# Performance work log

Hardware: AMD Instinct MI355X
Metric: run time of the kernel (lower is better)

The kernel has to match this reference:

```python
import jax, jax.numpy as jnp
import numpy as np

D_MODEL = 1024
N_HEADS = 16
D_K = D_MODEL // N_HEADS  # 64
SCALE = 0.125             # attention_scale = 1/sqrt(d_k)
ROPE_BASE = 10000.0
NEG_INF = -1e30


def setup_inputs() -> dict:
    key = jax.random.key(0)
    k1, k2, k3 = jax.random.split(key, 3)
    B, S = 2, 2048
    x = jax.random.normal(k1, (B, S, D_MODEL), jnp.float32)
    # torch Linear(d_model, 3*d_model, bias=False): stored here as [in, out]
    w_qkv = jax.random.normal(k2, (D_MODEL, 3 * D_MODEL), jnp.float32) * (D_MODEL ** -0.5)
    w_o = jax.random.normal(k3, (D_MODEL, D_MODEL), jnp.float32) * (D_MODEL ** -0.5)
    return {"x": x, "w_qkv": w_qkv, "w_o": w_o}


def _rotary(x):
    # x: [B, H, S, D]; standard half-split rotary over sequence positions
    S, D = x.shape[2], x.shape[3]
    inv_freq = 1.0 / (ROPE_BASE ** (jnp.arange(0, D, 2, dtype=jnp.float32) / D))  # [D/2]
    freqs = jnp.arange(S, dtype=jnp.float32)[:, None] * inv_freq[None, :]          # [S, D/2]
    cos = jnp.cos(freqs)[None, None]  # [1,1,S,D/2]
    sin = jnp.sin(freqs)[None, None]
    x1, x2 = jnp.split(x, 2, axis=-1)
    return jnp.concatenate([x1 * cos + x2 * sin, -x1 * sin + x2 * cos], axis=-1).astype(x.dtype)


def reference(x, w_qkv, w_o):
    B, S, _ = x.shape
    qkv = x @ w_qkv                                        # [B,S,3*D_MODEL]
    qkv = qkv.reshape(B, S, 3, N_HEADS, D_K).transpose(2, 0, 3, 1, 4)  # [3,B,H,S,Dk]
    q, k, v = qkv[0], qkv[1], qkv[2]
    q = _rotary(q)
    k = _rotary(k)
    scores = jnp.einsum('bhqd,bhkd->bhqk', q, k) * SCALE   # [B,H,S,S]
    causal = jnp.tril(jnp.ones((S, S), dtype=bool))
    scores = jnp.where(causal, scores, NEG_INF)
    attn = jax.nn.softmax(scores, axis=-1)
    out = jnp.einsum('bhqk,bhkd->bhqd', attn, v)           # [B,H,S,Dk]
    out = out.transpose(0, 2, 1, 3).reshape(B, S, D_MODEL)
    return out @ w_o
```

## Files before the change

kernel.cpp:

```cpp
#include <hip/hip_runtime.h>

typedef short bf16x8 __attribute__((ext_vector_type(8)));
typedef short bf16x4 __attribute__((ext_vector_type(4)));
typedef float f32x4 __attribute__((ext_vector_type(4)));
typedef float f32x16 __attribute__((ext_vector_type(16)));
typedef int i32x4 __attribute__((ext_vector_type(4)));

#define DEVI static __device__ __forceinline__

DEVI unsigned short f2b(float f) {
  unsigned u = __float_as_uint(f);
  u += 0x7FFFu + ((u >> 16) & 1u);
  return (unsigned short)(u >> 16);
}

DEVI void gload16(const void* g, void* l) {
  __builtin_amdgcn_global_load_lds((const __attribute__((address_space(1))) void*)g,
                                   (__attribute__((address_space(3))) void*)l, 16, 0, 0);
}

DEVI void pl32swap(int a, int b, int& outa, int& outb) {
#if __has_builtin(__builtin_amdgcn_permlane32_swap)
  auto r = __builtin_amdgcn_permlane32_swap(a, b, false, false);
  outa = ((const int*)&r)[0];
  outb = ((const int*)&r)[1];
#else
  int bp = __shfl_xor(b, 32);
  int ap = __shfl_xor(a, 32);
  outa = (threadIdx.x & 32) ? bp : a;
  outb = (threadIdx.x & 32) ? b : ap;
#endif
}

DEVI float halfmax(float x) {
  int o0, o1;
  pl32swap(__float_as_int(x), __float_as_int(x), o0, o1);
  return fmaxf(__int_as_float(o0), __int_as_float(o1));
}
DEVI float halfsum(float x) {
  int o0, o1;
  pl32swap(__float_as_int(x), __float_as_int(x), o0, o1);
  return __int_as_float(o0) + __int_as_float(o1);
}

__global__ void rope_table_kernel(float2* __restrict__ cst) {
  int i = blockIdx.x * 256 + threadIdx.x;
  int s = i >> 5, j = i & 31;
  float inv = powf(10000.0f, -(float)j * (1.0f / 32.0f));
  float a = (float)s * inv;
  cst[i] = make_float2(cosf(a), sinf(a));
}

__global__ void cvt_x_kernel(const float* __restrict__ x, unsigned short* __restrict__ xb) {
  int i = blockIdx.x * 256 + threadIdx.x;
  float4 v = ((const float4*)x)[i];
  ushort4 o;
  o.x = f2b(v.x); o.y = f2b(v.y); o.z = f2b(v.z); o.w = f2b(v.w);
  ((ushort4*)xb)[i] = o;
}

__global__ void transpose2_kernel(const float* __restrict__ W1, unsigned short* __restrict__ WT1,
                                  const float* __restrict__ W2, unsigned short* __restrict__ WT2) {
  __shared__ float tile[32][33];
  int bx = blockIdx.x;
  const float* W; unsigned short* WT; int N;
  if (bx < 96) { W = W1; WT = WT1; N = 3072; }
  else         { W = W2; WT = WT2; N = 1024; bx -= 96; }
  const int K = 1024;
  int n0 = bx * 32, k0 = blockIdx.y * 32;
  int tx = threadIdx.x, ty = threadIdx.y;
#pragma unroll
  for (int i = 0; i < 32; i += 8)
    tile[ty + i][tx] = W[(size_t)(k0 + ty + i) * N + n0 + tx];
  __syncthreads();
#pragma unroll
  for (int i = 0; i < 32; i += 8)
    WT[(size_t)(n0 + ty + i) * K + k0 + tx] = f2b(tile[tx][ty + i]);
}

DEVI void gemm_mainloop(const unsigned short* __restrict__ A, const unsigned short* __restrict__ B,
                        unsigned short* As, unsigned short* Bs,
                        int m0, int n0, int lane, int wid, int wr, int wc,
                        f32x4 acc[4][4]) {
  const int srow = lane >> 3;
  const int scc = ((lane & 7) ^ srow) * 8;
  const int rx = lane & 7;
  auto stage = [&](int k0, int nb) {
    unsigned short* Ad = As + nb * 8192;
    unsigned short* Bd = Bs + nb * 8192;
#pragma unroll
    for (int i = 0; i < 4; ++i) {
      const int c = i * 4 + wid;
      const int row = c * 8 + srow;
      gload16(A + (size_t)(m0 + row) * 1024 + k0 + scc, (char*)Ad + c * 1024);
      gload16(B + (size_t)(n0 + row) * 1024 + k0 + scc, (char*)Bd + c * 1024);
    }
  };
  auto compute = [&](int nb) {
    const unsigned short* Ab = As + nb * 8192;
    const unsigned short* Bb = Bs + nb * 8192;
#pragma unroll
    for (int kk = 0; kk < 64; kk += 32) {
      const int cc = (((kk >> 3) + (lane >> 4)) ^ rx) * 8;
      bf16x8 a[4], b[4];
#pragma unroll
      for (int mi = 0; mi < 4; ++mi)
        a[mi] = *(const bf16x8*)&Ab[(wr * 64 + mi * 16 + (lane & 15)) * 64 + cc];
#pragma unroll
      for (int ni = 0; ni < 4; ++ni)
        b[ni] = *(const bf16x8*)&Bb[(wc * 64 + ni * 16 + (lane & 15)) * 64 + cc];
      __builtin_amdgcn_s_setprio(1);
#pragma unroll
      for (int mi = 0; mi < 4; ++mi)
#pragma unroll
        for (int ni = 0; ni < 4; ++ni)
          acc[mi][ni] = __builtin_amdgcn_mfma_f32_16x16x32_bf16(a[mi], b[ni], acc[mi][ni], 0, 0, 0);
      __builtin_amdgcn_s_setprio(0);
    }
  };
  stage(0, 0);
  stage(64, 1);
  for (int t = 0; t < 15; ++t) {
    asm volatile("s_waitcnt vmcnt(8)" ::: "memory");
    __builtin_amdgcn_s_barrier();
    compute(t & 1);
    __builtin_amdgcn_s_barrier();
    if (t < 14) stage((t + 2) * 64, t & 1);
  }
  asm volatile("s_waitcnt vmcnt(0)" ::: "memory");
  __builtin_amdgcn_s_barrier();
  compute(1);
}

__global__ __launch_bounds__(256, 2) void gemm_qkv_kernel(
    const unsigned short* __restrict__ Xb, const unsigned short* __restrict__ WT,
    const float2* __restrict__ cst,
    unsigned short* __restrict__ Qb, unsigned short* __restrict__ Kb,
    unsigned short* __restrict__ VTb) {
  __shared__ unsigned short As[2][8192];
  __shared__ unsigned short Bs[2][8192];
  const int lane = threadIdx.x & 63, wid = threadIdx.x >> 6;
  const int flat = blockIdx.y * 24 + blockIdx.x;
  const int nf = (flat & 7) * 96 + (flat >> 3);
  const int bx = nf % 24, by = nf / 24;
  const int m0 = by * 128, n0 = bx * 128;
  const int wr = wid >> 1, wc = wid & 1;
  f32x4 acc[4][4] = {};
  gemm_mainloop(Xb, WT, &As[0][0], &Bs[0][0], m0, n0, lane, wid, wr, wc, acc);

  __syncthreads();
  unsigned short* slab = (unsigned short*)((char*)&As[0][0] + wid * 9216);
  const int n_base = n0 + wc * 64;
  const int ty = n_base >> 10;
  const int h = (n_base & 1023) >> 6;
  const int qrow = (lane >> 4) << 2;
  const int l15 = lane & 15;
  const int rlane = lane >> 3, clane = lane & 7;
  const int rowg = m0 + wr * 64;
  const int s_half = rowg & 2047, bb = rowg >> 11;

  if (ty < 2) {
    unsigned short* dst = (ty == 0) ? Qb : Kb;
#pragma unroll
    for (int mi = 0; mi < 4; ++mi) {
      const int rl0 = mi * 16 + qrow;
#pragma unroll
      for (int r = 0; r < 4; ++r) {
#pragma unroll
        for (int ni = 0; ni < 2; ++ni) {
          const int j = ni * 16 + l15;
          const float2 cs = cst[(s_half + rl0 + r) * 32 + j];
          const float x1 = acc[mi][ni][r], x2 = acc[mi][ni + 2][r];
          slab[(rl0 + r) * 72 + j]      = f2b(x1 * cs.x + x2 * cs.y);
          slab[(rl0 + r) * 72 + j + 32] = f2b(-x1 * cs.y + x2 * cs.x);
        }
      }
    }
    unsigned short* dp = dst + ((size_t)(bb * 16 + h) * 2048 + s_half) * 64;
#pragma unroll
    for (int i = 0; i < 8; ++i) {
      const int row = i * 8 + rlane;
      const bf16x8 v = *(const bf16x8*)&slab[row * 72 + clane * 8];
      *(bf16x8*)&dp[row * 64 + clane * 8] = v;
    }
  } else {
#pragma unroll
    for (int mi = 0; mi < 4; ++mi) {
      const int rl0 = mi * 16 + qrow;
#pragma unroll
      for (int ni = 0; ni < 4; ++ni) {
        const int d = ni * 16 + l15;
#pragma unroll
        for (int r = 0; r < 4; ++r)
          slab[d * 72 + rl0 + r] = f2b(acc[mi][ni][r]);
      }
    }
    unsigned short* vp = VTb + (size_t)(bb * 16 + h) * 64 * 2048 + s_half;
#pragma unroll
    for (int i = 0; i < 8; ++i) {
      const int d = i * 8 + rlane;
      const bf16x8 v = *(const bf16x8*)&slab[d * 72 + clane * 8];
      *(bf16x8*)&vp[(size_t)d * 2048 + clane * 8] = v;
    }
  }
}

DEVI void stage128(const unsigned short* __restrict__ Kh, const unsigned short* __restrict__ Vh,
                   int kbase, unsigned char* buf, int tid) {
#pragma unroll
  for (int i = 0; i < 4; ++i) {
    const int T = tid + i * 512;
    const int g = T >> 10;
    const int rem = T & 1023;
    const int cidx = rem & 511;
    const int c = cidx >> 6;
    const int l = cidx & 63;
    unsigned char* dst = buf + (T & ~63) * 16;
    if (rem < 512)
      gload16(Kh + (size_t)(kbase + g * 64 + l) * 64 + c * 8, dst);
    else
      gload16(Vh + (size_t)l * 2048 + kbase + g * 64 + c * 8, dst);
  }
}

DEVI void build_pa(const f32x16& s, bf16x8& pa0, bf16x8& pa1) {
  int cw[8];
#pragma unroll
  for (int i = 0; i < 8; ++i)
    asm("v_cvt_pk_bf16_f32 %0, %1, %2" : "=v"(cw[i]) : "v"(s[2 * i]), "v"(s[2 * i + 1]));
  int a0, a1, b0, b1, a2, a3, b2, b3;
  pl32swap(cw[0], cw[2], a0, b0);
  pl32swap(cw[1], cw[3], a1, b1);
  pl32swap(cw[4], cw[6], a2, b2);
  pl32swap(cw[5], cw[7], a3, b3);
  pa0 = __builtin_bit_cast(bf16x8, (i32x4){a0, a1, b0, b1});
  pa1 = __builtin_bit_cast(bf16x8, (i32x4){a2, a3, b2, b3});
}

DEVI void attn_pair(const unsigned char* __restrict__ bufK, const unsigned char* __restrict__ bufV,
                    const bf16x8 qf[4], int kglob, bool diag1, int qg, int ln, int hi,
                    float& m2, float& l_run, f32x16& acc0, f32x16& acc1) {
  const float C = 0.125f * 1.44269504f;
  f32x16 s0 = {}, s1 = {};
  {
    const unsigned char* kb = bufK + hi * 1024 + ln * 16;
    bf16x8 k0[4], k1[4];
#pragma unroll
    for (int j = 0; j < 4; ++j) {
      k0[j] = *(const bf16x8*)(kb + j * 2048);
      k1[j] = *(const bf16x8*)(kb + j * 2048 + 512);
    }
    __builtin_amdgcn_s_setprio(1);
#pragma unroll
    for (int j = 0; j < 4; ++j) {
      s0 = __builtin_amdgcn_mfma_f32_32x32x16_bf16(k0[j], qf[j], s0, 0, 0, 0);
      s1 = __builtin_amdgcn_mfma_f32_32x32x16_bf16(k1[j], qf[j], s1, 0, 0, 0);
    }
    __builtin_amdgcn_s_setprio(0);
  }
  bf16x8 va[2][2], vb[2][2];
  {
    const unsigned char* vbase = bufV + hi * 1024 + ln * 16;
#pragma unroll
    for (int st = 0; st < 2; ++st)
#pragma unroll
      for (int p = 0; p < 2; ++p) {
        va[st][p] = *(const bf16x8*)(vbase + (4 * st + 2 * p) * 1024);
        vb[st][p] = *(const bf16x8*)(vbase + (4 * st + 2 * p) * 1024 + 512);
      }
  }

  if (diag1) {
#pragma unroll
    for (int r = 0; r < 16; ++r) {
      const int kg = kglob + 32 + (r & 3) + ((r >> 2) << 3) + (hi << 2);
      if (kg > qg) s1[r] = -1e30f;
    }
  }
  float mraw = fmaxf(s0[0], s1[0]);
#pragma unroll
  for (int r = 1; r < 16; ++r) mraw = fmaxf(mraw, fmaxf(s0[r], s1[r]));
  const float mlc = mraw * C;
  if (__any(mlc > m2 + 11.5416f)) {
    const float mnew = fmaxf(m2, halfmax(mlc));
    const float sc = exp2f(m2 - mnew);
    l_run *= sc;
#pragma unroll
    for (int r = 0; r < 16; ++r) { acc0[r] *= sc; acc1[r] *= sc; }
    m2 = mnew;
  }
  float ps0 = 0.f, ps1 = 0.f;
#pragma unroll
  for (int r = 0; r < 16; ++r) { s0[r] = exp2f(fmaf(s0[r], C, -m2)); ps0 += s0[r]; }
#pragma unroll
  for (int r = 0; r < 16; ++r) { s1[r] = exp2f(fmaf(s1[r], C, -m2)); ps1 += s1[r]; }
  l_run += ps0 + ps1;

  bf16x8 pa[2][2];
  build_pa(s0, pa[0][0], pa[0][1]);
  build_pa(s1, pa[1][0], pa[1][1]);

  __builtin_amdgcn_s_setprio(1);
#pragma unroll
  for (int st = 0; st < 2; ++st) {
    acc0 = __builtin_amdgcn_mfma_f32_32x32x16_bf16(va[st][0], pa[st][0], acc0, 0, 0, 0);
    acc1 = __builtin_amdgcn_mfma_f32_32x32x16_bf16(vb[st][0], pa[st][0], acc1, 0, 0, 0);
    acc0 = __builtin_amdgcn_mfma_f32_32x32x16_bf16(va[st][1], pa[st][1], acc0, 0, 0, 0);
    acc1 = __builtin_amdgcn_mfma_f32_32x32x16_bf16(vb[st][1], pa[st][1], acc1, 0, 0, 0);
  }
  __builtin_amdgcn_s_setprio(0);
}

DEVI void attn_single(const unsigned char* __restrict__ bufK, const unsigned char* __restrict__ bufV,
                      const bf16x8 qf[4], int kglob, int qg, int ln, int hi,
                      float& m2, float& l_run, f32x16& acc0, f32x16& acc1) {
  const float C = 0.125f * 1.44269504f;
  f32x16 s0 = {};
  {
    const unsigned char* kb = bufK + hi * 1024 + ln * 16;
    bf16x8 k0[4];
#pragma unroll
    for (int j = 0; j < 4; ++j) k0[j] = *(const bf16x8*)(kb + j * 2048);
    __builtin_amdgcn_s_setprio(1);
#pragma unroll
    for (int j = 0; j < 4; ++j)
      s0 = __builtin_amdgcn_mfma_f32_32x32x16_bf16(k0[j], qf[j], s0, 0, 0, 0);
    __builtin_amdgcn_s_setprio(0);
  }
  bf16x8 va[2], vb[2];
  {
    const unsigned char* vbase = bufV + hi * 1024 + ln * 16;
#pragma unroll
    for (int p = 0; p < 2; ++p) {
      va[p] = *(const bf16x8*)(vbase + (2 * p) * 1024);
      vb[p] = *(const bf16x8*)(vbase + (2 * p) * 1024 + 512);
    }
  }
#pragma unroll
  for (int r = 0; r < 16; ++r) {
    const int kg = kglob + (r & 3) + ((r >> 2) << 3) + (hi << 2);
    if (kg > qg) s0[r] = -1e30f;
  }
  float mraw = s0[0];
#pragma unroll
  for (int r = 1; r < 16; ++r) mraw = fmaxf(mraw, s0[r]);
  const float mlc = mraw * C;
  if (__any(mlc > m2 + 11.5416f)) {
    const float mnew = fmaxf(m2, halfmax(mlc));
    const float sc = exp2f(m2 - mnew);
    l_run *= sc;
#pragma unroll
    for (int r = 0; r < 16; ++r) { acc0[r] *= sc; acc1[r] *= sc; }
    m2 = mnew;
  }
  float ps = 0.f;
#pragma unroll
  for (int r = 0; r < 16; ++r) { s0[r] = exp2f(fmaf(s0[r], C, -m2)); ps += s0[r]; }
  l_run += ps;

  bf16x8 pa0, pa1;
  build_pa(s0, pa0, pa1);
  __builtin_amdgcn_s_setprio(1);
  acc0 = __builtin_amdgcn_mfma_f32_32x32x16_bf16(va[0], pa0, acc0, 0, 0, 0);
  acc1 = __builtin_amdgcn_mfma_f32_32x32x16_bf16(vb[0], pa0, acc1, 0, 0, 0);
  acc0 = __builtin_amdgcn_mfma_f32_32x32x16_bf16(va[1], pa1, acc0, 0, 0, 0);
  acc1 = __builtin_amdgcn_mfma_f32_32x32x16_bf16(vb[1], pa1, acc1, 0, 0, 0);
  __builtin_amdgcn_s_setprio(0);
}

DEVI void write_partial(float* M, int slot, const f32x16& a0, const f32x16& a1,
                        float m2, float l) {
#pragma unroll
  for (int r = 0; r < 16; ++r) { M[slot + r] = a0[r]; M[slot + 16 + r] = a1[r]; }
  M[slot + 32] = m2;
  M[slot + 33] = l;
}

DEVI void write_merged(unsigned short* __restrict__ Ob, const float* M, int slot,
                       const f32x16& acc0, const f32x16& acc1, float m2, float l_run,
                       int bh, int q0, int ln, int hi) {
  const float mp = M[slot + 32], lp = M[slot + 33];
  const float m = fmaxf(m2, mp);
  const float eo = exp2f(m2 - m), ep = exp2f(mp - m);
  const float il = 1.0f / (l_run * eo + lp * ep);
  const int b = bh >> 4, h = bh & 15;
  unsigned short* ob = Ob + ((size_t)(b * 2048 + q0 + ln)) * 1024 + h * 64;
#pragma unroll
  for (int g = 0; g < 4; ++g) {
    ushort4 o0, o1;
    o0.x = f2b((acc0[4 * g + 0] * eo + M[slot + 4 * g + 0] * ep) * il);
    o0.y = f2b((acc0[4 * g + 1] * eo + M[slot + 4 * g + 1] * ep) * il);
    o0.z = f2b((acc0[4 * g + 2] * eo + M[slot + 4 * g + 2] * ep) * il);
    o0.w = f2b((acc0[4 * g + 3] * eo + M[slot + 4 * g + 3] * ep) * il);
    o1.x = f2b((acc1[4 * g + 0] * eo + M[slot + 16 + 4 * g + 0] * ep) * il);
    o1.y = f2b((acc1[4 * g + 1] * eo + M[slot + 16 + 4 * g + 1] * ep) * il);
    o1.z = f2b((acc1[4 * g + 2] * eo + M[slot + 16 + 4 * g + 2] * ep) * il);
    o1.w = f2b((acc1[4 * g + 3] * eo + M[slot + 16 + 4 * g + 3] * ep) * il);
    *(ushort4*)&ob[8 * g + 4 * hi]      = o0;
    *(ushort4*)&ob[32 + 8 * g + 4 * hi] = o1;
  }
}

__global__ __launch_bounds__(512, 2) void attn_kernel(
    const unsigned short* __restrict__ Qb, const unsigned short* __restrict__ Kb,
    const unsigned short* __restrict__ VTb, unsigned short* __restrict__ Ob) {
  __shared__ unsigned char smem[2][2][16384];
  const int tid = threadIdx.x;
  const int lane = tid & 63, wid = tid >> 6;
  const int ln = lane & 31, hi = lane >> 5;
  const int s = wid & 3, half = wid >> 2;
  const int bh = blockIdx.x;
  const int p = blockIdx.y;
  const int jA = 15 - p, jB = p;
  const unsigned short* Qh = Qb + (size_t)bh * 2048 * 64;
  const unsigned short* Kh = Kb + (size_t)bh * 2048 * 64;
  const unsigned short* Vh = VTb + (size_t)bh * 64 * 2048;

  f32x16 aA0 = {}, aA1 = {}, aB0 = {}, aB1 = {};
  float mA = -1e30f, lA = 0.f, mB = -1e30f, lB = 0.f;
  int it = 0;

  auto load_q = [&](int q0, bf16x8 qf[4]) {
    const unsigned short* pq = Qh + (size_t)(q0 + ln) * 64 + hi * 8;
#pragma unroll
    for (int t = 0; t < 4; ++t) qf[t] = *(const bf16x8*)(pq + t * 16);
  };
  auto run_phase = [&](int j, const bf16x8 qf[4], f32x16& acc0, f32x16& acc1,
                       float& m2, float& l_run, int q0, int nextFirst) {
    const int qg = q0 + ln;
    const int top = q0 >> 5;
    for (int kb = 0; kb <= j; ++kb, ++it) {
      const int nxt = (kb < j) ? (kb + 1) * 128 : nextFirst;
      if (nxt >= 0) stage128(Kh, Vh, nxt, &smem[(it + 1) & 1][0][0], tid);
      const unsigned char* bufK = &smem[it & 1][half][0];
      const unsigned char* bufV = bufK + 8192;
      const int t64 = 2 * kb + half;
      const int nv = top - 2 * t64 + 1;
      if (nv >= 2)
        attn_pair(bufK, bufV, qf, t64 * 64, top == 2 * t64 + 1, qg, ln, hi,
                  m2, l_run, acc0, acc1);
      else if (nv == 1)
        attn_single(bufK, bufV, qf, t64 * 64, qg, ln, hi, m2, l_run, acc0, acc1);
      __syncthreads();
    }
  };

  bf16x8 qfA[4];
  load_q(jA * 128 + s * 32, qfA);
  stage128(Kh, Vh, 0, &smem[0][0][0], tid);
  __syncthreads();
  run_phase(jA, qfA, aA0, aA1, mA, lA, jA * 128 + s * 32, 0);
  bf16x8 qfB[4];
  load_q(jB * 128 + s * 32, qfB);
  run_phase(jB, qfB, aB0, aB1, mB, lB, jB * 128 + s * 32, -1);

  lA = halfsum(lA);
  lB = halfsum(lB);

  float* M = (float*)&smem[0][0][0];
  const int slot = (s * 64 + lane) * 34;
  if (half == 1) write_partial(M, slot, aA0, aA1, mA, lA);
  __syncthreads();
  if (half == 0) write_merged(Ob, M, slot, aA0, aA1, mA, lA, bh, jA * 128 + s * 32, ln, hi);
  __syncthreads();
  if (half == 0) write_partial(M, slot, aB0, aB1, mB, lB);
  __syncthreads();
  if (half == 1) write_merged(Ob, M, slot, aB0, aB1, mB, lB, bh, jB * 128 + s * 32, ln, hi);
}

__global__ __launch_bounds__(256) void gemm_out_kernel(
    const unsigned short* __restrict__ Ob, const unsigned short* __restrict__ WoT,
    float* __restrict__ out) {
  __shared__ unsigned short As[2][8192];
  __shared__ unsigned short Bs[2][8192];
  const int lane = threadIdx.x & 63, wid = threadIdx.x >> 6;
  const int m0 = blockIdx.y * 128, n0 = blockIdx.x * 128;
  const int wr = wid >> 1, wc = wid & 1;
  f32x4 acc[4][4] = {};
  gemm_mainloop(Ob, WoT, &As[0][0], &Bs[0][0], m0, n0, lane, wid, wr, wc, acc);
#pragma unroll
  for (int mi = 0; mi < 4; ++mi) {
    const int mrow = m0 + wr * 64 + mi * 16 + ((lane >> 4) << 2);
#pragma unroll
    for (int ni = 0; ni < 4; ++ni) {
      const int n = n0 + wc * 64 + ni * 16 + (lane & 15);
#pragma unroll
      for (int r = 0; r < 4; ++r)
        out[(size_t)(mrow + r) * 1024 + n] = acc[mi][ni][r];
    }
  }
}

extern "C" void kernel_launch(void* const* d_in, const int* in_sizes, int n_in,
                              void* d_out, int out_size, void* d_ws, size_t ws_size,
                              hipStream_t stream) {
  const float* x     = (const float*)d_in[0];
  const float* w_qkv = (const float*)d_in[1];
  const float* w_o   = (const float*)d_in[2];
  float* out = (float*)d_out;
  char* ws = (char*)d_ws;

  const size_t MB = 1 << 20;
  float2* cst = (float2*)(ws);
  unsigned short* Xb  = (unsigned short*)(ws + (512 << 10));
  unsigned short* WqT = (unsigned short*)(ws + (512 << 10) + 8  * MB);
  unsigned short* WoT = (unsigned short*)(ws + (512 << 10) + 14 * MB);
  unsigned short* Qb  = (unsigned short*)(ws + (512 << 10) + 16 * MB);
  unsigned short* Kb  = (unsigned short*)(ws + (512 << 10) + 24 * MB);
  unsigned short* VTb = (unsigned short*)(ws + (512 << 10) + 32 * MB);
  unsigned short* Ob  = Xb;

  rope_table_kernel<<<dim3(256), dim3(256), 0, stream>>>(cst);
  cvt_x_kernel<<<dim3(4096), dim3(256), 0, stream>>>(x, Xb);
  transpose2_kernel<<<dim3(128, 32), dim3(32, 8), 0, stream>>>(w_qkv, WqT, w_o, WoT);
  gemm_qkv_kernel<<<dim3(24, 32), dim3(256), 0, stream>>>(Xb, WqT, cst, Qb, Kb, VTb);
  attn_kernel<<<dim3(32, 8), dim3(512), 0, stream>>>(Qb, Kb, VTb, Ob);
  gemm_out_kernel<<<dim3(8, 32), dim3(256), 0, stream>>>(Ob, WoT, out);
}
```

Baseline: 120.7 us.

## Pre-tile K/V in fragment layout and read directly from global in attention

The QKV GEMM epilogue now writes K and V into a per-64-key tiled layout that matches the MFMA fragment order. The attention kernel drops its LDS double-buffered staging and reads K/V fragments straight from global memory (L2). Each 8-wave block now splits its waves so that each half handles its own query tile over all keys, instead of both halves sharing key tiles and merging partial softmax state through LDS. This removes LDS traffic, barriers and the merge step, but every wave now fetches K/V from global memory on its own, which relies on the cache and adds latency that is not hidden by prefetching.

```diff
diff --git a/kernel.cpp b/kernel.cpp
--- a/kernel.cpp
+++ b/kernel.cpp
@@ -135,8 +135,8 @@
 __global__ __launch_bounds__(256, 2) void gemm_qkv_kernel(
     const unsigned short* __restrict__ Xb, const unsigned short* __restrict__ WT,
     const float2* __restrict__ cst,
-    unsigned short* __restrict__ Qb, unsigned short* __restrict__ Kb,
-    unsigned short* __restrict__ VTb) {
+    unsigned short* __restrict__ Qb, unsigned short* __restrict__ KT,
+    unsigned short* __restrict__ VT) {
   __shared__ unsigned short As[2][8192];
   __shared__ unsigned short Bs[2][8192];
   const int lane = threadIdx.x & 63, wid = threadIdx.x >> 6;
@@ -149,18 +149,18 @@
   gemm_mainloop(Xb, WT, &As[0][0], &Bs[0][0], m0, n0, lane, wid, wr, wc, acc);
 
   __syncthreads();
-  unsigned short* slab = (unsigned short*)((char*)&As[0][0] + wid * 9216);
+  unsigned short* slab = (unsigned short*)((char*)&As[0][0] + wid * 8192);
   const int n_base = n0 + wc * 64;
   const int ty = n_base >> 10;
   const int h = (n_base & 1023) >> 6;
   const int qrow = (lane >> 4) << 2;
   const int l15 = lane & 15;
-  const int rlane = lane >> 3, clane = lane & 7;
   const int rowg = m0 + wr * 64;
   const int s_half = rowg & 2047, bb = rowg >> 11;
-
-  if (ty < 2) {
-    unsigned short* dst = (ty == 0) ? Qb : Kb;
+  const int t_ = s_half >> 6;
+  const size_t hb = (size_t)(bb * 16 + h) * 131072;
+
+  if (ty == 0) {
 #pragma unroll
     for (int mi = 0; mi < 4; ++mi) {
       const int rl0 = mi * 16 + qrow;
@@ -171,55 +171,61 @@
           const int j = ni * 16 + l15;
           const float2 cs = cst[(s_half + rl0 + r) * 32 + j];
           const float x1 = acc[mi][ni][r], x2 = acc[mi][ni + 2][r];
-          slab[(rl0 + r) * 72 + j]      = f2b(x1 * cs.x + x2 * cs.y);
-          slab[(rl0 + r) * 72 + j + 32] = f2b(-x1 * cs.y + x2 * cs.x);
+          slab[(rl0 + r) * 64 + j]      = f2b(x1 * cs.x + x2 * cs.y);
+          slab[(rl0 + r) * 64 + j + 32] = f2b(-x1 * cs.y + x2 * cs.x);
         }
       }
     }
-    unsigned short* dp = dst + ((size_t)(bb * 16 + h) * 2048 + s_half) * 64;
+    unsigned short* dst = Qb + hb + (size_t)s_half * 64;
 #pragma unroll
     for (int i = 0; i < 8; ++i) {
-      const int row = i * 8 + rlane;
-      const bf16x8 v = *(const bf16x8*)&slab[row * 72 + clane * 8];
-      *(bf16x8*)&dp[row * 64 + clane * 8] = v;
-    }
-  } else {
+      const int idx = i * 64 + lane;
+      *(bf16x8*)&dst[idx * 8] = *(const bf16x8*)&slab[idx * 8];
+    }
+  } else if (ty == 1) {
 #pragma unroll
     for (int mi = 0; mi < 4; ++mi) {
       const int rl0 = mi * 16 + qrow;
 #pragma unroll
+      for (int r = 0; r < 4; ++r) {
+        const int row = rl0 + r;
+#pragma unroll
+        for (int ni = 0; ni < 2; ++ni) {
+          const int j = ni * 16 + l15;
+          const float2 cs = cst[(s_half + row) * 32 + j];
+          const float x1 = acc[mi][ni][r], x2 = acc[mi][ni + 2][r];
+          const int c = j >> 3, jr = j & 7;
+          slab[c * 512 + row * 8 + jr]       = f2b(x1 * cs.x + x2 * cs.y);
+          slab[(c + 4) * 512 + row * 8 + jr] = f2b(-x1 * cs.y + x2 * cs.x);
+        }
+      }
+    }
+    unsigned short* dst = KT + hb + (size_t)t_ * 4096;
+#pragma unroll
+    for (int i = 0; i < 8; ++i) {
+      const int idx = i * 64 + lane;
+      *(bf16x8*)&dst[idx * 8] = *(const bf16x8*)&slab[idx * 8];
+    }
+  } else {
+#pragma unroll
+    for (int mi = 0; mi < 4; ++mi) {
+      const int rl0 = mi * 16 + qrow;
+#pragma unroll
       for (int ni = 0; ni < 4; ++ni) {
         const int d = ni * 16 + l15;
 #pragma unroll
-        for (int r = 0; r < 4; ++r)
-          slab[d * 72 + rl0 + r] = f2b(acc[mi][ni][r]);
+        for (int r = 0; r < 4; ++r) {
+          const int rl = rl0 + r;
+          slab[(rl >> 3) * 512 + d * 8 + (rl & 7)] = f2b(acc[mi][ni][r]);
+        }
       }
     }
-    unsigned short* vp = VTb + (size_t)(bb * 16 + h) * 64 * 2048 + s_half;
+    unsigned short* dst = VT + hb + (size_t)t_ * 4096;
 #pragma unroll
     for (int i = 0; i < 8; ++i) {
-      const int d = i * 8 + rlane;
-      const bf16x8 v = *(const bf16x8*)&slab[d * 72 + clane * 8];
-      *(bf16x8*)&vp[(size_t)d * 2048 + clane * 8] = v;
-    }
-  }
-}
-
-DEVI void stage128(const unsigned short* __restrict__ Kh, const unsigned short* __restrict__ Vh,
-                   int kbase, unsigned char* buf, int tid) {
-#pragma unroll
-  for (int i = 0; i < 4; ++i) {
-    const int T = tid + i * 512;
-    const int g = T >> 10;
-    const int rem = T & 1023;
-    const int cidx = rem & 511;
-    const int c = cidx >> 6;
-    const int l = cidx & 63;
-    unsigned char* dst = buf + (T & ~63) * 16;
-    if (rem < 512)
-      gload16(Kh + (size_t)(kbase + g * 64 + l) * 64 + c * 8, dst);
-    else
-      gload16(Vh + (size_t)l * 2048 + kbase + g * 64 + c * 8, dst);
+      const int idx = i * 64 + lane;
+      *(bf16x8*)&dst[idx * 8] = *(const bf16x8*)&slab[idx * 8];
+    }
   }
 }
 
@@ -237,18 +243,18 @@
   pa1 = __builtin_bit_cast(bf16x8, (i32x4){a2, a3, b2, b3});
 }
 
-DEVI void attn_pair(const unsigned char* __restrict__ bufK, const unsigned char* __restrict__ bufV,
+DEVI void attn_pair(const unsigned char* __restrict__ kb, const unsigned char* __restrict__ vb,
                     const bf16x8 qf[4], int kglob, bool diag1, int qg, int ln, int hi,
                     float& m2, float& l_run, f32x16& acc0, f32x16& acc1) {
   const float C = 0.125f * 1.44269504f;
   f32x16 s0 = {}, s1 = {};
   {
-    const unsigned char* kb = bufK + hi * 1024 + ln * 16;
+    const unsigned char* kbase = kb + hi * 1024 + ln * 16;
     bf16x8 k0[4], k1[4];
 #pragma unroll
     for (int j = 0; j < 4; ++j) {
-      k0[j] = *(const bf16x8*)(kb + j * 2048);
-      k1[j] = *(const bf16x8*)(kb + j * 2048 + 512);
+      k0[j] = *(const bf16x8*)(kbase + j * 2048);
+      k1[j] = *(const bf16x8*)(kbase + j * 2048 + 512);
     }
     __builtin_amdgcn_s_setprio(1);
 #pragma unroll
@@ -258,15 +264,15 @@
     }
     __builtin_amdgcn_s_setprio(0);
   }
-  bf16x8 va[2][2], vb[2][2];
+  bf16x8 va[2][2], vbf[2][2];
   {
-    const unsigned char* vbase = bufV + hi * 1024 + ln * 16;
+    const unsigned char* vbase = vb + hi * 1024 + ln * 16;
 #pragma unroll
     for (int st = 0; st < 2; ++st)
 #pragma unroll
       for (int p = 0; p < 2; ++p) {
-        va[st][p] = *(const bf16x8*)(vbase + (4 * st + 2 * p) * 1024);
-        vb[st][p] = *(const bf16x8*)(vbase + (4 * st + 2 * p) * 1024 + 512);
+        va[st][p]  = *(const bf16x8*)(vbase + (4 * st + 2 * p) * 1024);
+        vbf[st][p] = *(const bf16x8*)(vbase + (4 * st + 2 * p) * 1024 + 512);
       }
   }
 
@@ -304,36 +310,36 @@
 #pragma unroll
   for (int st = 0; st < 2; ++st) {
     acc0 = __builtin_amdgcn_mfma_f32_32x32x16_bf16(va[st][0], pa[st][0], acc0, 0, 0, 0);
-    acc1 = __builtin_amdgcn_mfma_f32_32x32x16_bf16(vb[st][0], pa[st][0], acc1, 0, 0, 0);
+    acc1 = __builtin_amdgcn_mfma_f32_32x32x16_bf16(vbf[st][0], pa[st][0], acc1, 0, 0, 0);
     acc0 = __builtin_amdgcn_mfma_f32_32x32x16_bf16(va[st][1], pa[st][1], acc0, 0, 0, 0);
-    acc1 = __builtin_amdgcn_mfma_f32_32x32x16_bf16(vb[st][1], pa[st][1], acc1, 0, 0, 0);
+    acc1 = __builtin_amdgcn_mfma_f32_32x32x16_bf16(vbf[st][1], pa[st][1], acc1, 0, 0, 0);
   }
   __builtin_amdgcn_s_setprio(0);
 }
 
-DEVI void attn_single(const unsigned char* __restrict__ bufK, const unsigned char* __restrict__ bufV,
+DEVI void attn_single(const unsigned char* __restrict__ kb, const unsigned char* __restrict__ vb,
                       const bf16x8 qf[4], int kglob, int qg, int ln, int hi,
                       float& m2, float& l_run, f32x16& acc0, f32x16& acc1) {
   const float C = 0.125f * 1.44269504f;
   f32x16 s0 = {};
   {
-    const unsigned char* kb = bufK + hi * 1024 + ln * 16;
+    const unsigned char* kbase = kb + hi * 1024 + ln * 16;
     bf16x8 k0[4];
 #pragma unroll
-    for (int j = 0; j < 4; ++j) k0[j] = *(const bf16x8*)(kb + j * 2048);
+    for (int j = 0; j < 4; ++j) k0[j] = *(const bf16x8*)(kbase + j * 2048);
     __builtin_amdgcn_s_setprio(1);
 #pragma unroll
     for (int j = 0; j < 4; ++j)
       s0 = __builtin_amdgcn_mfma_f32_32x32x16_bf16(k0[j], qf[j], s0, 0, 0, 0);
     __builtin_amdgcn_s_setprio(0);
   }
-  bf16x8 va[2], vb[2];
+  bf16x8 va[2], vbf[2];
   {
-    const unsigned char* vbase = bufV + hi * 1024 + ln * 16;
+    const unsigned char* vbase = vb + hi * 1024 + ln * 16;
 #pragma unroll
     for (int p = 0; p < 2; ++p) {
-      va[p] = *(const bf16x8*)(vbase + (2 * p) * 1024);
-      vb[p] = *(const bf16x8*)(vbase + (2 * p) * 1024 + 512);
+      va[p]  = *(const bf16x8*)(vbase + (2 * p) * 1024);
+      vbf[p] = *(const bf16x8*)(vbase + (2 * p) * 1024 + 512);
     }
   }
 #pragma unroll
@@ -362,110 +368,64 @@
   build_pa(s0, pa0, pa1);
   __builtin_amdgcn_s_setprio(1);
   acc0 = __builtin_amdgcn_mfma_f32_32x32x16_bf16(va[0], pa0, acc0, 0, 0, 0);
-  acc1 = __builtin_amdgcn_mfma_f32_32x32x16_bf16(vb[0], pa0, acc1, 0, 0, 0);
+  acc1 = __builtin_amdgcn_mfma_f32_32x32x16_bf16(vbf[0], pa0, acc1, 0, 0, 0);
   acc0 = __builtin_amdgcn_mfma_f32_32x32x16_bf16(va[1], pa1, acc0, 0, 0, 0);
-  acc1 = __builtin_amdgcn_mfma_f32_32x32x16_bf16(vb[1], pa1, acc1, 0, 0, 0);
+  acc1 = __builtin_amdgcn_mfma_f32_32x32x16_bf16(vbf[1], pa1, acc1, 0, 0, 0);
   __builtin_amdgcn_s_setprio(0);
 }
 
-DEVI void write_partial(float* M, int slot, const f32x16& a0, const f32x16& a1,
-                        float m2, float l) {
-#pragma unroll
-  for (int r = 0; r < 16; ++r) { M[slot + r] = a0[r]; M[slot + 16 + r] = a1[r]; }
-  M[slot + 32] = m2;
-  M[slot + 33] = l;
-}
-
-DEVI void write_merged(unsigned short* __restrict__ Ob, const float* M, int slot,
-                       const f32x16& acc0, const f32x16& acc1, float m2, float l_run,
-                       int bh, int q0, int ln, int hi) {
-  const float mp = M[slot + 32], lp = M[slot + 33];
-  const float m = fmaxf(m2, mp);
-  const float eo = exp2f(m2 - m), ep = exp2f(mp - m);
-  const float il = 1.0f / (l_run * eo + lp * ep);
-  const int b = bh >> 4, h = bh & 15;
-  unsigned short* ob = Ob + ((size_t)(b * 2048 + q0 + ln)) * 1024 + h * 64;
-#pragma unroll
-  for (int g = 0; g < 4; ++g) {
-    ushort4 o0, o1;
-    o0.x = f2b((acc0[4 * g + 0] * eo + M[slot + 4 * g + 0] * ep) * il);
-    o0.y = f2b((acc0[4 * g + 1] * eo + M[slot + 4 * g + 1] * ep) * il);
-    o0.z = f2b((acc0[4 * g + 2] * eo + M[slot + 4 * g + 2] * ep) * il);
-    o0.w = f2b((acc0[4 * g + 3] * eo + M[slot + 4 * g + 3] * ep) * il);
-    o1.x = f2b((acc1[4 * g + 0] * eo + M[slot + 16 + 4 * g + 0] * ep) * il);
-    o1.y = f2b((acc1[4 * g + 1] * eo + M[slot + 16 + 4 * g + 1] * ep) * il);
-    o1.z = f2b((acc1[4 * g + 2] * eo + M[slot + 16 + 4 * g + 2] * ep) * il);
-    o1.w = f2b((acc1[4 * g + 3] * eo + M[slot + 16 + 4 * g + 3] * ep) * il);
-    *(ushort4*)&ob[8 * g + 4 * hi]      = o0;
-    *(ushort4*)&ob[32 + 8 * g + 4 * hi] = o1;
-  }
-}
-
 __global__ __launch_bounds__(512, 2) void attn_kernel(
-    const unsigned short* __restrict__ Qb, const unsigned short* __restrict__ Kb,
-    const unsigned short* __restrict__ VTb, unsigned short* __restrict__ Ob) {
-  __shared__ unsigned char smem[2][2][16384];
+    const unsigned short* __restrict__ Qb, const unsigned short* __restrict__ KT,
+    const unsigned short* __restrict__ VT, unsigned short* __restrict__ Ob) {
   const int tid = threadIdx.x;
   const int lane = tid & 63, wid = tid >> 6;
   const int ln = lane & 31, hi = lane >> 5;
   const int s = wid & 3, half = wid >> 2;
   const int bh = blockIdx.x;
   const int p = blockIdx.y;
-  const int jA = 15 - p, jB = p;
-  const unsigned short* Qh = Qb + (size_t)bh * 2048 * 64;
-  const unsigned short* Kh = Kb + (size_t)bh * 2048 * 64;
-  const unsigned short* Vh = VTb + (size_t)bh * 64 * 2048;
-
-  f32x16 aA0 = {}, aA1 = {}, aB0 = {}, aB1 = {};
-  float mA = -1e30f, lA = 0.f, mB = -1e30f, lB = 0.f;
-  int it = 0;
-
-  auto load_q = [&](int q0, bf16x8 qf[4]) {
+  const int j = half ? p : (15 - p);
+  const int q0 = j * 128 + s * 32;
+  const int qg = q0 + ln;
+  const int top = q0 >> 5;
+  const unsigned short* Qh = Qb + (size_t)bh * 131072;
+  const unsigned char* KTb = (const unsigned char*)(KT + (size_t)bh * 131072);
+  const unsigned char* VTb = (const unsigned char*)(VT + (size_t)bh * 131072);
+
+  bf16x8 qf[4];
+  {
     const unsigned short* pq = Qh + (size_t)(q0 + ln) * 64 + hi * 8;
 #pragma unroll
     for (int t = 0; t < 4; ++t) qf[t] = *(const bf16x8*)(pq + t * 16);
-  };
-  auto run_phase = [&](int j, const bf16x8 qf[4], f32x16& acc0, f32x16& acc1,
-                       float& m2, float& l_run, int q0, int nextFirst) {
-    const int qg = q0 + ln;
-    const int top = q0 >> 5;
-    for (int kb = 0; kb <= j; ++kb, ++it) {
-      const int nxt = (kb < j) ? (kb + 1) * 128 : nextFirst;
-      if (nxt >= 0) stage128(Kh, Vh, nxt, &smem[(it + 1) & 1][0][0], tid);
-      const unsigned char* bufK = &smem[it & 1][half][0];
-      const unsigned char* bufV = bufK + 8192;
-      const int t64 = 2 * kb + half;
-      const int nv = top - 2 * t64 + 1;
-      if (nv >= 2)
-        attn_pair(bufK, bufV, qf, t64 * 64, top == 2 * t64 + 1, qg, ln, hi,
-                  m2, l_run, acc0, acc1);
-      else if (nv == 1)
-        attn_single(bufK, bufV, qf, t64 * 64, qg, ln, hi, m2, l_run, acc0, acc1);
-      __syncthreads();
-    }
-  };
-
-  bf16x8 qfA[4];
-  load_q(jA * 128 + s * 32, qfA);
-  stage128(Kh, Vh, 0, &smem[0][0][0], tid);
-  __syncthreads();
-  run_phase(jA, qfA, aA0, aA1, mA, lA, jA * 128 + s * 32, 0);
-  bf16x8 qfB[4];
-  load_q(jB * 128 + s * 32, qfB);
-  run_phase(jB, qfB, aB0, aB1, mB, lB, jB * 128 + s * 32, -1);
-
-  lA = halfsum(lA);
-  lB = halfsum(lB);
-
-  float* M = (float*)&smem[0][0][0];
-  const int slot = (s * 64 + lane) * 34;
-  if (half == 1) write_partial(M, slot, aA0, aA1, mA, lA);
-  __syncthreads();
-  if (half == 0) write_merged(Ob, M, slot, aA0, aA1, mA, lA, bh, jA * 128 + s * 32, ln, hi);
-  __syncthreads();
-  if (half == 0) write_partial(M, slot, aB0, aB1, mB, lB);
-  __syncthreads();
-  if (half == 1) write_merged(Ob, M, slot, aB0, aB1, mB, lB, bh, jB * 128 + s * 32, ln, hi);
+  }
+
+  f32x16 acc0 = {}, acc1 = {};
+  float m2 = -1e30f, l_run = 0.f;
+  const int ntile = (top >> 1) + 1;
+
+  for (int t = 0; t < ntile; ++t) {
+    const unsigned char* kb = KTb + (size_t)t * 8192;
+    const unsigned char* vb = VTb + (size_t)t * 8192;
+    const int nv = top - 2 * t + 1;
+    if (nv >= 2)
+      attn_pair(kb, vb, qf, t * 64, top == 2 * t + 1, qg, ln, hi, m2, l_run, acc0, acc1);
+    else
+      attn_single(kb, vb, qf, t * 64, qg, ln, hi, m2, l_run, acc0, acc1);
+  }
+  l_run = halfsum(l_run);
+
+  const float il = 1.0f / l_run;
+  const int b = bh >> 4, h = bh & 15;
+  unsigned short* ob = Ob + ((size_t)(b * 2048 + qg)) * 1024 + h * 64;
+#pragma unroll
+  for (int g = 0; g < 4; ++g) {
+    ushort4 o0, o1;
+    o0.x = f2b(acc0[4 * g + 0] * il); o0.y = f2b(acc0[4 * g + 1] * il);
+    o0.z = f2b(acc0[4 * g + 2] * il); o0.w = f2b(acc0[4 * g + 3] * il);
+    o1.x = f2b(acc1[4 * g + 0] * il); o1.y = f2b(acc1[4 * g + 1] * il);
+    o1.z = f2b(acc1[4 * g + 2] * il); o1.w = f2b(acc1[4 * g + 3] * il);
+    *(ushort4*)&ob[8 * g + 4 * hi]      = o0;
+    *(ushort4*)&ob[32 + 8 * g + 4 * hi] = o1;
+  }
 }
 
 __global__ __launch_bounds__(256) void gemm_out_kernel(
@@ -506,14 +466,14 @@
   unsigned short* WqT = (unsigned short*)(ws + (512 << 10) + 8  * MB);
   unsigned short* WoT = (unsigned short*)(ws + (512 << 10) + 14 * MB);
   unsigned short* Qb  = (unsigned short*)(ws + (512 << 10) + 16 * MB);
-  unsigned short* Kb  = (unsigned short*)(ws + (512 << 10) + 24 * MB);
-  unsigned short* VTb = (unsigned short*)(ws + (512 << 10) + 32 * MB);
+  unsigned short* KT  = (unsigned short*)(ws + (512 << 10) + 24 * MB);
+  unsigned short* VT  = (unsigned short*)(ws + (512 << 10) + 32 * MB);
   unsigned short* Ob  = Xb;
 
   rope_table_kernel<<<dim3(256), dim3(256), 0, stream>>>(cst);
   cvt_x_kernel<<<dim3(4096), dim3(256), 0, stream>>>(x, Xb);
   transpose2_kernel<<<dim3(128, 32), dim3(32, 8), 0, stream>>>(w_qkv, WqT, w_o, WoT);
-  gemm_qkv_kernel<<<dim3(24, 32), dim3(256), 0, stream>>>(Xb, WqT, cst, Qb, Kb, VTb);
-  attn_kernel<<<dim3(32, 8), dim3(512), 0, stream>>>(Qb, Kb, VTb, Ob);
+  gemm_qkv_kernel<<<dim3(24, 32), dim3(256), 0, stream>>>(Xb, WqT, cst, Qb, KT, VT);
+  attn_kernel<<<dim3(32, 8), dim3(512), 0, stream>>>(Qb, KT, VT, Ob);
   gemm_out_kernel<<<dim3(8, 32), dim3(256), 0, stream>>>(Ob, WoT, out);
 }
```

New measurement: 123.5 us. 1.02x slower.

## Share K/V tile loads between both query blocks in a single attention loop

Applied to the files above, without the earlier changes.

Merges the two sequential per-query-block phases into one loop over key blocks. Each staged K/V tile is now used by both query blocks A and B, so the kernel no longer re-stages the first jB+1 key blocks and needs fewer barriers. Both Q fragment sets and both accumulator sets stay live at the same time, which raises register pressure, so the launch bound drops its minimum-occupancy hint of 2 blocks.

```diff
diff --git a/kernel.cpp b/kernel.cpp
--- a/kernel.cpp
+++ b/kernel.cpp
@@ -401,7 +401,7 @@
   }
 }
 
-__global__ __launch_bounds__(512, 2) void attn_kernel(
+__global__ __launch_bounds__(512) void attn_kernel(
     const unsigned short* __restrict__ Qb, const unsigned short* __restrict__ Kb,
     const unsigned short* __restrict__ VTb, unsigned short* __restrict__ Ob) {
   __shared__ unsigned char smem[2][2][16384];
@@ -418,41 +418,42 @@
 
   f32x16 aA0 = {}, aA1 = {}, aB0 = {}, aB1 = {};
   float mA = -1e30f, lA = 0.f, mB = -1e30f, lB = 0.f;
-  int it = 0;
 
   auto load_q = [&](int q0, bf16x8 qf[4]) {
     const unsigned short* pq = Qh + (size_t)(q0 + ln) * 64 + hi * 8;
 #pragma unroll
     for (int t = 0; t < 4; ++t) qf[t] = *(const bf16x8*)(pq + t * 16);
   };
-  auto run_phase = [&](int j, const bf16x8 qf[4], f32x16& acc0, f32x16& acc1,
-                       float& m2, float& l_run, int q0, int nextFirst) {
-    const int qg = q0 + ln;
-    const int top = q0 >> 5;
-    for (int kb = 0; kb <= j; ++kb, ++it) {
-      const int nxt = (kb < j) ? (kb + 1) * 128 : nextFirst;
-      if (nxt >= 0) stage128(Kh, Vh, nxt, &smem[(it + 1) & 1][0][0], tid);
-      const unsigned char* bufK = &smem[it & 1][half][0];
-      const unsigned char* bufV = bufK + 8192;
-      const int t64 = 2 * kb + half;
-      const int nv = top - 2 * t64 + 1;
-      if (nv >= 2)
-        attn_pair(bufK, bufV, qf, t64 * 64, top == 2 * t64 + 1, qg, ln, hi,
-                  m2, l_run, acc0, acc1);
-      else if (nv == 1)
-        attn_single(bufK, bufV, qf, t64 * 64, qg, ln, hi, m2, l_run, acc0, acc1);
-      __syncthreads();
-    }
-  };
-
-  bf16x8 qfA[4];
-  load_q(jA * 128 + s * 32, qfA);
+  bf16x8 qfA[4], qfB[4];
+  const int q0A = jA * 128 + s * 32, q0B = jB * 128 + s * 32;
+  load_q(q0A, qfA);
+  load_q(q0B, qfB);
+  const int qgA = q0A + ln, qgB = q0B + ln;
+  const int topA = q0A >> 5, topB = q0B >> 5;
+
   stage128(Kh, Vh, 0, &smem[0][0][0], tid);
   __syncthreads();
-  run_phase(jA, qfA, aA0, aA1, mA, lA, jA * 128 + s * 32, 0);
-  bf16x8 qfB[4];
-  load_q(jB * 128 + s * 32, qfB);
-  run_phase(jB, qfB, aB0, aB1, mB, lB, jB * 128 + s * 32, -1);
+  for (int kb = 0; kb <= jA; ++kb) {
+    if (kb < jA) stage128(Kh, Vh, (kb + 1) * 128, &smem[(kb + 1) & 1][0][0], tid);
+    const unsigned char* bufK = &smem[kb & 1][half][0];
+    const unsigned char* bufV = bufK + 8192;
+    const int t64 = 2 * kb + half;
+    {
+      const int nv = topA - 2 * t64 + 1;
+      if (nv >= 2)
+        attn_pair(bufK, bufV, qfA, t64 * 64, topA == 2 * t64 + 1, qgA, ln, hi, mA, lA, aA0, aA1);
+      else if (nv == 1)
+        attn_single(bufK, bufV, qfA, t64 * 64, qgA, ln, hi, mA, lA, aA0, aA1);
+    }
+    {
+      const int nv = topB - 2 * t64 + 1;
+      if (nv >= 2)
+        attn_pair(bufK, bufV, qfB, t64 * 64, topB == 2 * t64 + 1, qgB, ln, hi, mB, lB, aB0, aB1);
+      else if (nv == 1)
+        attn_single(bufK, bufV, qfB, t64 * 64, qgB, ln, hi, mB, lB, aB0, aB1);
+    }
+    __syncthreads();
+  }
 
   lA = halfsum(lA);
   lB = halfsum(lB);
@@ -461,11 +462,11 @@
   const int slot = (s * 64 + lane) * 34;
   if (half == 1) write_partial(M, slot, aA0, aA1, mA, lA);
   __syncthreads();
-  if (half == 0) write_merged(Ob, M, slot, aA0, aA1, mA, lA, bh, jA * 128 + s * 32, ln, hi);
+  if (half == 0) write_merged(Ob, M, slot, aA0, aA1, mA, lA, bh, q0A, ln, hi);
   __syncthreads();
   if (half == 0) write_partial(M, slot, aB0, aB1, mB, lB);
   __syncthreads();
-  if (half == 1) write_merged(Ob, M, slot, aB0, aB1, mB, lB, bh, jB * 128 + s * 32, ln, hi);
+  if (half == 1) write_merged(Ob, M, slot, aB0, aB1, mB, lB, bh, q0B, ln, hi);
 }
 
 __global__ __launch_bounds__(256) void gemm_out_kernel(
```

Result: no change. 120.8 us (+0.0%).
